# Kernel optimization log

Hardware: AMD Instinct MI355X
Metric: run time of the kernel (lower is better)

Reference implementation:

```python
import jax, jax.numpy as jnp
import numpy as np

NUM_HEADS = 16
HEAD_DIM = 32  # out_ch 512 / 16 heads

def _c(x):
    # last axis holds (real, imag) -> complex64
    return jax.lax.complex(x[..., 0], x[..., 1])

def setup_inputs() -> dict:
    key = jax.random.key(0)
    ks = jax.random.split(key, 9)
    B, S, C = 1, 2048, 512
    mk = lambda k, shp: jax.random.normal(k, shp, dtype=jnp.float32)
    return {
        "Q": mk(ks[0], (B, S, C, 2)),
        "V": mk(ks[1], (B, S, C, 2)),
        "K": mk(ks[2], (B, S, C, 2)),
        "Wq": mk(ks[3], (C, C, 2)) * (1.0 / np.sqrt(C)),
        "bq": mk(ks[4], (C, 2)) * 0.02,
        "Wk": mk(ks[5], (C, C, 2)) * (1.0 / np.sqrt(C)),
        "bk": mk(ks[6], (C, 2)) * 0.02,
        "Wv": mk(ks[7], (C, C, 2)) * (1.0 / np.sqrt(C)),
        "bv": mk(ks[8], (C, 2)) * 0.02,
    }

def _split_heads(x):
    B, S, D = x.shape
    return x.reshape(B, S, NUM_HEADS, HEAD_DIM).transpose(0, 2, 1, 3)  # [B,H,S,d]

def reference(Q, V, K, Wq, bq, Wk, bk, Wv, bv):
    Qc, Kc, Vc = _c(Q), _c(K), _c(V)
    # torch Linear: y = x @ W^T + b, W is [out, in]
    proj = lambda x, W, b: jnp.einsum('bsi,oi->bso', x, _c(W)) + _c(b)
    q = _split_heads(proj(Qc, Wq, bq))  # [B,H,S,d] complex64
    k = _split_heads(proj(Kc, Wk, bk))
    v = _split_heads(proj(Vc, Wv, bv))
    scores = jnp.einsum('bhqd,bhkd->bhqk', q, jnp.conj(k)) / np.sqrt(HEAD_DIM).astype(np.float32)
    weights = jax.nn.softmax(jnp.abs(scores), axis=-1)  # real [B,H,S,S]
    out = jnp.einsum('bhqk,bhkd->bhqd', weights.astype(v.dtype), v)  # complex
    B, H, S, d = out.shape
    out = out.transpose(0, 2, 1, 3).reshape(B, S, H * d)  # [B,S,out_ch]
    return jnp.stack([out.real, out.imag], axis=-1)  # [B,S,out_ch,2] float32
```

## Files before the change

### kernel.cpp

```cpp
#include <hip/hip_runtime.h>
#include <hip/hip_bf16.h>
#include <math.h>

#define S_LEN 2048
#define C_DIM 512
#define NH 16
#define HD 32
#define PLANE_U (NH * S_LEN * HD)

typedef __attribute__((ext_vector_type(8)))  short bf16x8;
typedef __attribute__((ext_vector_type(8)))  unsigned short u16x8;
typedef __attribute__((ext_vector_type(4)))  float f32x4;
typedef __attribute__((ext_vector_type(16))) float f32x16;
typedef __attribute__((ext_vector_type(4)))  unsigned int u32x4;

#if __has_builtin(__builtin_amdgcn_exp2f)
#define EXP2(x) __builtin_amdgcn_exp2f(x)
#else
#define EXP2(x) exp2f(x)
#endif

__device__ __forceinline__ unsigned int pk_bf16(float a, float b) {
    float2 f; f.x = a; f.y = b;
    __hip_bfloat162 t = __float22bfloat162_rn(f);
    return *reinterpret_cast<unsigned int*>(&t);
}

#define PROW 40

__global__ __launch_bounds__(256)
void proj_mfma(const float* __restrict__ Q, const float* __restrict__ V,
               const float* __restrict__ K,
               const float* __restrict__ Wq, const float* __restrict__ bq,
               const float* __restrict__ Wk, const float* __restrict__ bk,
               const float* __restrict__ Wv, const float* __restrict__ bv,
               unsigned short* __restrict__ ws)
{
    const int z = blockIdx.z;
    const float *X, *W, *b;
    if (z == 0)      { X = Q; W = Wq; b = bq; }
    else if (z == 1) { X = K; W = Wk; b = bk; }
    else             { X = V; W = Wv; b = bv; }
    const bool full = (z < 2);

    const int s0 = blockIdx.x * 64;
    const int o0 = blockIdx.y * 64;

    const float2 *Asrc, *Bsrc; int arow0, brow0;
    if (full) { Asrc = (const float2*)W; arow0 = o0; Bsrc = (const float2*)X; brow0 = s0; }
    else      { Asrc = (const float2*)X; arow0 = s0; Bsrc = (const float2*)W; brow0 = o0; }

    __shared__ __align__(16) unsigned short LBrh[64*PROW], LBrl[64*PROW];
    __shared__ __align__(16) unsigned short LBih[64*PROW], LBil[64*PROW];

    const int t    = threadIdx.x;
    const int wave = t >> 6;
    const int lr   = t & 15;
    const int g    = (t & 63) >> 4;
    const int srow = t >> 2;
    const int sk8  = (t & 3) * 8;

    const f32x4 zf = {0.f,0.f,0.f,0.f};
    f32x4 accR[4], accI[4];
    #pragma unroll
    for (int i = 0; i < 4; ++i) { accR[i] = zf; accI[i] = zf; }

    const float4* Arow4 = (const float4*)(Asrc + (size_t)(arow0 + wave*16 + lr)*C_DIM);

    for (int k0 = 0; k0 < C_DIM; k0 += 32) {
        const float4* a4 = Arow4 + ((k0 + g*8) >> 1);
        float4 A0 = a4[0], A1 = a4[1], A2 = a4[2], A3 = a4[3];

        __syncthreads();
        {
            const float4* s4 = (const float4*)(Bsrc + (size_t)(brow0 + srow)*C_DIM + k0 + sk8);
            float4 f0 = s4[0], f1 = s4[1], f2v = s4[2], f3 = s4[3];
            float re[8] = {f0.x,f0.z,f1.x,f1.z,f2v.x,f2v.z,f3.x,f3.z};
            float im[8] = {f0.y,f0.w,f1.y,f1.w,f2v.y,f2v.w,f3.y,f3.w};
            u32x4 rh, ih, rl, il;
            if (full) {
                #pragma unroll
                for (int p2 = 0; p2 < 4; ++p2) {
                    float r0f = re[2*p2], r1f = re[2*p2+1];
                    float i0f = im[2*p2], i1f = im[2*p2+1];
                    unsigned int br0 = __float_as_uint(r0f), br1 = __float_as_uint(r1f);
                    unsigned int bi0 = __float_as_uint(i0f), bi1 = __float_as_uint(i1f);
                    rh[p2] = __builtin_amdgcn_perm(br1, br0, 0x07060302u);
                    ih[p2] = __builtin_amdgcn_perm(bi1, bi0, 0x07060302u);
                    rl[p2] = pk_bf16(r0f - __uint_as_float(br0 & 0xFFFF0000u),
                                     r1f - __uint_as_float(br1 & 0xFFFF0000u));
                    il[p2] = pk_bf16(i0f - __uint_as_float(bi0 & 0xFFFF0000u),
                                     i1f - __uint_as_float(bi1 & 0xFFFF0000u));
                }
            } else {
                #pragma unroll
                for (int p2 = 0; p2 < 4; ++p2) {
                    rh[p2] = pk_bf16(re[2*p2], re[2*p2+1]);
                    ih[p2] = pk_bf16(im[2*p2], im[2*p2+1]);
                }
            }
            int wb = srow*PROW + sk8;
            *(u32x4*)&LBrh[wb] = rh; *(u32x4*)&LBih[wb] = ih;
            if (full) { *(u32x4*)&LBrl[wb] = rl; *(u32x4*)&LBil[wb] = il; }
        }

        bf16x8 aRH, aIH, aRL, aIL;
        {
            float re[8] = {A0.x,A0.z,A1.x,A1.z,A2.x,A2.z,A3.x,A3.z};
            float im[8] = {A0.y,A0.w,A1.y,A1.w,A2.y,A2.w,A3.y,A3.w};
            u32x4 rh, ih, rl, il;
            if (full) {
                #pragma unroll
                for (int p2 = 0; p2 < 4; ++p2) {
                    float r0f = re[2*p2], r1f = re[2*p2+1];
                    float i0f = im[2*p2], i1f = im[2*p2+1];
                    unsigned int br0 = __float_as_uint(r0f), br1 = __float_as_uint(r1f);
                    unsigned int bi0 = __float_as_uint(i0f), bi1 = __float_as_uint(i1f);
                    rh[p2] = __builtin_amdgcn_perm(br1, br0, 0x07060302u);
                    ih[p2] = __builtin_amdgcn_perm(bi1, bi0, 0x07060302u);
                    rl[p2] = pk_bf16(r0f - __uint_as_float(br0 & 0xFFFF0000u),
                                     r1f - __uint_as_float(br1 & 0xFFFF0000u));
                    il[p2] = pk_bf16(i0f - __uint_as_float(bi0 & 0xFFFF0000u),
                                     i1f - __uint_as_float(bi1 & 0xFFFF0000u));
                }
                aRL = *(bf16x8*)&rl; aIL = *(bf16x8*)&il;
            } else {
                #pragma unroll
                for (int p2 = 0; p2 < 4; ++p2) {
                    rh[p2] = pk_bf16(re[2*p2], re[2*p2+1]);
                    ih[p2] = pk_bf16(im[2*p2], im[2*p2+1]);
                }
            }
            aRH = *(bf16x8*)&rh; aIH = *(bf16x8*)&ih;
        }
        bf16x8 aIHn;
        #pragma unroll
        for (int j = 0; j < 8; ++j) aIHn[j] = aIH[j] ^ (short)0x8000;

        __syncthreads();

        if (full) {
            bf16x8 aILn;
            #pragma unroll
            for (int j = 0; j < 8; ++j) aILn[j] = aIL[j] ^ (short)0x8000;

            #pragma unroll
            for (int tile = 0; tile < 4; ++tile) {
                const int bb = (tile*16 + lr)*PROW + g*8;
                bf16x8 bRH = *(const bf16x8*)&LBrh[bb];
                bf16x8 bRL = *(const bf16x8*)&LBrl[bb];
                bf16x8 bIH = *(const bf16x8*)&LBih[bb];
                bf16x8 bIL = *(const bf16x8*)&LBil[bb];
                accR[tile] = __builtin_amdgcn_mfma_f32_16x16x32_bf16(aRH,  bRH, accR[tile], 0,0,0);
                accR[tile] = __builtin_amdgcn_mfma_f32_16x16x32_bf16(aRL,  bRH, accR[tile], 0,0,0);
                accR[tile] = __builtin_amdgcn_mfma_f32_16x16x32_bf16(aRH,  bRL, accR[tile], 0,0,0);
                accR[tile] = __builtin_amdgcn_mfma_f32_16x16x32_bf16(aIHn, bIH, accR[tile], 0,0,0);
                accR[tile] = __builtin_amdgcn_mfma_f32_16x16x32_bf16(aILn, bIH, accR[tile], 0,0,0);
                accR[tile] = __builtin_amdgcn_mfma_f32_16x16x32_bf16(aIHn, bIL, accR[tile], 0,0,0);
                accI[tile] = __builtin_amdgcn_mfma_f32_16x16x32_bf16(aRH,  bIH, accI[tile], 0,0,0);
                accI[tile] = __builtin_amdgcn_mfma_f32_16x16x32_bf16(aRL,  bIH, accI[tile], 0,0,0);
                accI[tile] = __builtin_amdgcn_mfma_f32_16x16x32_bf16(aRH,  bIL, accI[tile], 0,0,0);
                accI[tile] = __builtin_amdgcn_mfma_f32_16x16x32_bf16(aIH,  bRH, accI[tile], 0,0,0);
                accI[tile] = __builtin_amdgcn_mfma_f32_16x16x32_bf16(aIL,  bRH, accI[tile], 0,0,0);
                accI[tile] = __builtin_amdgcn_mfma_f32_16x16x32_bf16(aIH,  bRL, accI[tile], 0,0,0);
            }
        } else {
            #pragma unroll
            for (int tile = 0; tile < 4; ++tile) {
                const int bb = (tile*16 + lr)*PROW + g*8;
                bf16x8 bRH = *(const bf16x8*)&LBrh[bb];
                bf16x8 bIH = *(const bf16x8*)&LBih[bb];
                accR[tile] = __builtin_amdgcn_mfma_f32_16x16x32_bf16(aRH,  bRH, accR[tile], 0,0,0);
                accR[tile] = __builtin_amdgcn_mfma_f32_16x16x32_bf16(aIHn, bIH, accR[tile], 0,0,0);
                accI[tile] = __builtin_amdgcn_mfma_f32_16x16x32_bf16(aRH,  bIH, accI[tile], 0,0,0);
                accI[tile] = __builtin_amdgcn_mfma_f32_16x16x32_bf16(aIH,  bRH, accI[tile], 0,0,0);
            }
        }
    }

    const float2* b2 = (const float2*)b;
    if (z == 0) {
        const float osc = 0.2550348677f;
        unsigned short* pr = ws;
        unsigned short* pi = pr + PLANE_U;
        const int obase = o0 + wave*16 + g*4;
        const int hh = obase >> 5, d0 = obase & 31;
        float bR[4], bI[4];
        #pragma unroll
        for (int r = 0; r < 4; ++r) { float2 bb = b2[obase + r]; bR[r] = bb.x; bI[r] = bb.y; }
        #pragma unroll
        for (int tile = 0; tile < 4; ++tile) {
            int s = s0 + tile*16 + lr;
            size_t idx = ((size_t)hh*S_LEN + s)*HD + d0;
            uint2 pkR, pkI;
            pkR.x = pk_bf16((accR[tile][0]+bR[0])*osc, (accR[tile][1]+bR[1])*osc);
            pkR.y = pk_bf16((accR[tile][2]+bR[2])*osc, (accR[tile][3]+bR[3])*osc);
            pkI.x = pk_bf16((accI[tile][0]+bI[0])*osc, (accI[tile][1]+bI[1])*osc);
            pkI.y = pk_bf16((accI[tile][2]+bI[2])*osc, (accI[tile][3]+bI[3])*osc);
            *(uint2*)&pr[idx] = pkR;
            *(uint2*)&pi[idx] = pkI;
        }
    } else if (z == 1) {
        unsigned short* kf = ws + 2*(size_t)PLANE_U;
        const int obase = o0 + wave*16 + g*4;
        const int hh = obase >> 5, d0 = obase & 31;
        const int frag_re = (d0 >= 16) ? 1 : 0;
        const int bsel    = (d0 & 15) >> 3;
        const int e       = d0 & 7;
        float bR[4], bI[4];
        #pragma unroll
        for (int r = 0; r < 4; ++r) { float2 bb = b2[obase + r]; bR[r] = bb.x; bI[r] = bb.y; }
        #pragma unroll
        for (int tile = 0; tile < 4; ++tile) {
            int s = s0 + tile*16 + lr;
            int c = s >> 5;
            int i = s & 31;
            int r = (i & ~12) | ((i & 4) << 1) | ((i & 8) >> 1);
            int lane = bsel*32 + r;
            size_t base = ((size_t)(hh*64 + c)*4)*512 + lane*8 + e;
            uint2 pkR, pkI;
            pkR.x = pk_bf16(accR[tile][0]+bR[0], accR[tile][1]+bR[1]);
            pkR.y = pk_bf16(accR[tile][2]+bR[2], accR[tile][3]+bR[3]);
            pkI.x = pk_bf16(accI[tile][0]+bI[0], accI[tile][1]+bI[1]);
            pkI.y = pk_bf16(accI[tile][2]+bI[2], accI[tile][3]+bI[3]);
            *(uint2*)&kf[base + (size_t)frag_re*512]       = pkR;
            *(uint2*)&kf[base + (size_t)(2+frag_re)*512]   = pkI;
        }
    } else {
        unsigned short* vf = ws + 4*(size_t)PLANE_U;
        const int sbase = s0 + wave*16 + g*4;
        const int c  = sbase >> 5;
        const int j0 = sbase & 31;
        const int frag_re = (j0 >= 16) ? 1 : 0;
        const int bsel    = (j0 & 15) >> 3;
        const int e       = j0 & 7;
        #pragma unroll
        for (int tile = 0; tile < 4; ++tile) {
            int o = o0 + tile*16 + lr;
            int hh = o >> 5, d = o & 31;
            float2 bb = b2[o];
            int lane = bsel*32 + d;
            size_t base = ((size_t)(hh*64 + c)*4)*512 + lane*8 + e;
            uint2 pkR, pkI;
            pkR.x = pk_bf16(accR[tile][0]+bb.x, accR[tile][1]+bb.x);
            pkR.y = pk_bf16(accR[tile][2]+bb.x, accR[tile][3]+bb.x);
            pkI.x = pk_bf16(accI[tile][0]+bb.y, accI[tile][1]+bb.y);
            pkI.y = pk_bf16(accI[tile][2]+bb.y, accI[tile][3]+bb.y);
            *(uint2*)&vf[base + (size_t)frag_re*512]       = pkR;
            *(uint2*)&vf[base + (size_t)(2+frag_re)*512]   = pkI;
        }
    }
}

#define RROW 33

__global__ __launch_bounds__(256, 4)
void attn_mfma(const unsigned short* __restrict__ ws, float* __restrict__ out)
{
    const int bid   = blockIdx.x;
    const int h     = bid & (NH - 1);
    const int qblk  = bid >> 4;
    const int wave  = threadIdx.x >> 6;
    const int l     = threadIdx.x & 63;
    const int q     = l & 31;
    const int b     = l >> 5;

    const unsigned short* qr = ws + 0*(size_t)PLANE_U + (size_t)h*S_LEN*HD;
    const unsigned short* qi = ws + 1*(size_t)PLANE_U + (size_t)h*S_LEN*HD;
    const unsigned short* kf = ws + 2*(size_t)PLANE_U + ((size_t)h << 17);
    const unsigned short* vf = ws + 4*(size_t)PLANE_U + ((size_t)h << 17);

    const int q0 = qblk * 32;

    bf16x8 bQr_lo = *(const bf16x8*)&qr[(size_t)(q0 + q)*HD + b*8];
    bf16x8 bQr_hi = *(const bf16x8*)&qr[(size_t)(q0 + q)*HD + 16 + b*8];
    bf16x8 bQi_lo = *(const bf16x8*)&qi[(size_t)(q0 + q)*HD + b*8];
    bf16x8 bQi_hi = *(const bf16x8*)&qi[(size_t)(q0 + q)*HD + 16 + b*8];

    __shared__ __align__(16) float2 red[2*32*RROW];

    f32x16 accR, accI;
    #pragma unroll
    for (int r = 0; r < 16; ++r) { accR[r] = 0.f; accI[r] = 0.f; }
    float lsum = 0.f;

    const f32x16 z16 = {0,0,0,0,0,0,0,0,0,0,0,0,0,0,0,0};
    const int kbeg = wave * 512;
    for (int k0 = kbeg; k0 < kbeg + 512; k0 += 32) {
        const size_t fb = (size_t)(k0 >> 5) * 2048 + l*8;

        bf16x8 aVr_lo = *(const bf16x8*)&vf[fb];
        bf16x8 aVr_hi = *(const bf16x8*)&vf[fb + 512];
        bf16x8 aVi_lo = *(const bf16x8*)&vf[fb + 1024];
        bf16x8 aVi_hi = *(const bf16x8*)&vf[fb + 1536];

        bf16x8 aKr_lo = *(const bf16x8*)&kf[fb];
        bf16x8 aKr_hi = *(const bf16x8*)&kf[fb + 512];
        bf16x8 aKi_lo = *(const bf16x8*)&kf[fb + 1024];
        bf16x8 aKi_hi = *(const bf16x8*)&kf[fb + 1536];
        bf16x8 aKin_lo, aKin_hi;
        #pragma unroll
        for (int j = 0; j < 4; ++j) {
            ((unsigned int*)&aKin_lo)[j] = ((const unsigned int*)&aKi_lo)[j] ^ 0x80008000u;
            ((unsigned int*)&aKin_hi)[j] = ((const unsigned int*)&aKi_hi)[j] ^ 0x80008000u;
        }
        f32x16 sR = __builtin_amdgcn_mfma_f32_32x32x16_bf16(aKr_lo,  bQr_lo, z16, 0, 0, 0);
        f32x16 sI = __builtin_amdgcn_mfma_f32_32x32x16_bf16(aKin_lo, bQr_lo, z16, 0, 0, 0);
        sR = __builtin_amdgcn_mfma_f32_32x32x16_bf16(aKr_hi,  bQr_hi, sR, 0, 0, 0);
        sI = __builtin_amdgcn_mfma_f32_32x32x16_bf16(aKin_hi, bQr_hi, sI, 0, 0, 0);
        sR = __builtin_amdgcn_mfma_f32_32x32x16_bf16(aKi_lo,  bQi_lo, sR, 0, 0, 0);
        sI = __builtin_amdgcn_mfma_f32_32x32x16_bf16(aKr_lo,  bQi_lo, sI, 0, 0, 0);
        sR = __builtin_amdgcn_mfma_f32_32x32x16_bf16(aKi_hi,  bQi_hi, sR, 0, 0, 0);
        sI = __builtin_amdgcn_mfma_f32_32x32x16_bf16(aKr_hi,  bQi_hi, sI, 0, 0, 0);
        bf16x8 bP1, bP2;
        unsigned int* p1 = (unsigned int*)&bP1;
        unsigned int* p2 = (unsigned int*)&bP2;
        #pragma unroll
        for (int r2 = 0; r2 < 8; ++r2) {
            int r = 2*r2;
            float v0 = EXP2(__builtin_amdgcn_sqrtf(fmaf(sR[r],   sR[r],   sI[r]*sI[r])));
            float v1 = EXP2(__builtin_amdgcn_sqrtf(fmaf(sR[r+1], sR[r+1], sI[r+1]*sI[r+1])));
            lsum += v0 + v1;
            if (r2 < 4) p1[r2]     = pk_bf16(v0, v1);
            else        p2[r2 - 4] = pk_bf16(v0, v1);
        }
        accR = __builtin_amdgcn_mfma_f32_32x32x16_bf16(aVr_lo, bP1, accR, 0, 0, 0);
        accI = __builtin_amdgcn_mfma_f32_32x32x16_bf16(aVi_lo, bP1, accI, 0, 0, 0);
        accR = __builtin_amdgcn_mfma_f32_32x32x16_bf16(aVr_hi, bP2, accR, 0, 0, 0);
        accI = __builtin_amdgcn_mfma_f32_32x32x16_bf16(aVi_hi, bP2, accI, 0, 0, 0);
    }

    lsum += __shfl_xor(lsum, 32);

    const int rrow = ((wave & 1) * 32 + q) * RROW;
    __syncthreads();
    if (wave < 2) {
        #pragma unroll
        for (int r = 0; r < 16; ++r) {
            int d = (r & 3) + 8*(r >> 2) + 4*b;
            red[rrow + d] = make_float2(accR[r], accI[r]);
        }
        if (b == 0) red[rrow + 32].x = lsum;
    }
    __syncthreads();
    if (wave >= 2) {
        #pragma unroll
        for (int r = 0; r < 16; ++r) {
            int d = (r & 3) + 8*(r >> 2) + 4*b;
            float2 v = red[rrow + d];
            v.x += accR[r]; v.y += accI[r];
            red[rrow + d] = v;
        }
        if (b == 0) red[rrow + 32].x += lsum;
    }
    __syncthreads();

    {
        const int i  = threadIdx.x;
        const int oq = i >> 3;
        const int d0 = (i & 7) * 4;
        float sl = red[oq*RROW + 32].x + red[(32 + oq)*RROW + 32].x;
        float inv = 1.0f / sl;
        float2* o2 = (float2*)out;
        #pragma unroll
        for (int dd = 0; dd < 4; ++dd) {
            int d = d0 + dd;
            float2 v0 = red[oq*RROW + d];
            float2 v1 = red[(32 + oq)*RROW + d];
            o2[(size_t)(q0 + oq)*C_DIM + h*HD + d] =
                make_float2((v0.x + v1.x)*inv, (v0.y + v1.y)*inv);
        }
    }
}

extern "C" void kernel_launch(void* const* d_in, const int* in_sizes, int n_in,
                              void* d_out, int out_size, void* d_ws, size_t ws_size,
                              hipStream_t stream)
{
    const float* Q  = (const float*)d_in[0];
    const float* V  = (const float*)d_in[1];
    const float* K  = (const float*)d_in[2];
    const float* Wq = (const float*)d_in[3];
    const float* bq = (const float*)d_in[4];
    const float* Wk = (const float*)d_in[5];
    const float* bk = (const float*)d_in[6];
    const float* Wv = (const float*)d_in[7];
    const float* bv = (const float*)d_in[8];
    unsigned short* ws = (unsigned short*)d_ws;
    float* out = (float*)d_out;

    dim3 gp(S_LEN/64, C_DIM/64, 3);
    proj_mfma<<<gp, 256, 0, stream>>>(Q, V, K, Wq, bq, Wk, bk, Wv, bv, ws);

    attn_mfma<<<dim3(64*NH), 256, 0, stream>>>(ws, out);
}
```

Measured before the change: 81.72 us.

## Pre-convert weights to bf16 split planes and shrink projection seq tile

Adds a separate kernel that converts Wq/Wk/Wv into bf16 hi/lo planes once per call, so the projection kernel loads ready-made MFMA operands instead of re-splitting fp32 weights in every block. The projection's sequence tile drops from 64 to 32 rows, doubling the block count. The V projection now always uses weights as the A operand, which changes its output scatter to scalar 16-bit stores. The cost is an extra launch, extra workspace traffic, and less reuse of each weight fetch per block.

```diff
diff --git a/kernel.cpp b/kernel.cpp
--- a/kernel.cpp
+++ b/kernel.cpp
@@ -7,12 +7,14 @@
 #define NH 16
 #define HD 32
 #define PLANE_U (NH * S_LEN * HD)
+#define WPL 262144
 
 typedef __attribute__((ext_vector_type(8)))  short bf16x8;
 typedef __attribute__((ext_vector_type(8)))  unsigned short u16x8;
 typedef __attribute__((ext_vector_type(4)))  float f32x4;
 typedef __attribute__((ext_vector_type(16))) float f32x16;
 typedef __attribute__((ext_vector_type(4)))  unsigned int u32x4;
+typedef __attribute__((ext_vector_type(2)))  unsigned int u32x2;
 
 #if __has_builtin(__builtin_amdgcn_exp2f)
 #define EXP2(x) __builtin_amdgcn_exp2f(x)
@@ -26,61 +28,118 @@
     return *reinterpret_cast<unsigned int*>(&t);
 }
 
+__global__ __launch_bounds__(256)
+void wcvt(const float* __restrict__ Wq, const float* __restrict__ Wk,
+          const float* __restrict__ Wv, unsigned short* __restrict__ ws)
+{
+    const int tid = blockIdx.x*256 + threadIdx.x;
+    const int z   = tid >> 15;
+    const int rem = tid & 32767;
+    const int row = rem >> 6;
+    const int kc  = (rem & 63) * 8;
+    const float2* w2 = (const float2*)(z == 0 ? Wq : (z == 1 ? Wk : Wv));
+    const float4* s4 = (const float4*)(w2 + (size_t)row*C_DIM + kc);
+    float4 f0 = s4[0], f1 = s4[1], f2v = s4[2], f3 = s4[3];
+    float re[8] = {f0.x,f0.z,f1.x,f1.z,f2v.x,f2v.z,f3.x,f3.z};
+    float im[8] = {f0.y,f0.w,f1.y,f1.w,f2v.y,f2v.w,f3.y,f3.w};
+    unsigned short* wf = ws + 6*(size_t)PLANE_U;
+    const size_t off = (size_t)row*C_DIM + kc;
+    if (z < 2) {
+        u32x4 rh, ih, rl, il;
+        #pragma unroll
+        for (int p2 = 0; p2 < 4; ++p2) {
+            float r0f = re[2*p2], r1f = re[2*p2+1];
+            float i0f = im[2*p2], i1f = im[2*p2+1];
+            unsigned int br0 = __float_as_uint(r0f), br1 = __float_as_uint(r1f);
+            unsigned int bi0 = __float_as_uint(i0f), bi1 = __float_as_uint(i1f);
+            rh[p2] = __builtin_amdgcn_perm(br1, br0, 0x07060302u);
+            ih[p2] = __builtin_amdgcn_perm(bi1, bi0, 0x07060302u);
+            rl[p2] = pk_bf16(r0f - __uint_as_float(br0 & 0xFFFF0000u),
+                             r1f - __uint_as_float(br1 & 0xFFFF0000u));
+            il[p2] = pk_bf16(i0f - __uint_as_float(bi0 & 0xFFFF0000u),
+                             i1f - __uint_as_float(bi1 & 0xFFFF0000u));
+        }
+        const size_t pb = (size_t)z*4*WPL;
+        *(u32x4*)&wf[pb + 0*WPL + off] = rh;
+        *(u32x4*)&wf[pb + 1*WPL + off] = rl;
+        *(u32x4*)&wf[pb + 2*WPL + off] = ih;
+        *(u32x4*)&wf[pb + 3*WPL + off] = il;
+    } else {
+        u32x4 rh, ih;
+        #pragma unroll
+        for (int p2 = 0; p2 < 4; ++p2) {
+            rh[p2] = pk_bf16(re[2*p2], re[2*p2+1]);
+            ih[p2] = pk_bf16(im[2*p2], im[2*p2+1]);
+        }
+        *(u32x4*)&wf[(size_t)8*WPL + off] = rh;
+        *(u32x4*)&wf[(size_t)9*WPL + off] = ih;
+    }
+}
+
 #define PROW 40
 
 __global__ __launch_bounds__(256)
 void proj_mfma(const float* __restrict__ Q, const float* __restrict__ V,
                const float* __restrict__ K,
-               const float* __restrict__ Wq, const float* __restrict__ bq,
-               const float* __restrict__ Wk, const float* __restrict__ bk,
-               const float* __restrict__ Wv, const float* __restrict__ bv,
+               const float* __restrict__ bq, const float* __restrict__ bk,
+               const float* __restrict__ bv,
                unsigned short* __restrict__ ws)
 {
     const int z = blockIdx.z;
-    const float *X, *W, *b;
-    if (z == 0)      { X = Q; W = Wq; b = bq; }
-    else if (z == 1) { X = K; W = Wk; b = bk; }
-    else             { X = V; W = Wv; b = bv; }
+    const float *X, *b;
+    if (z == 0)      { X = Q; b = bq; }
+    else if (z == 1) { X = K; b = bk; }
+    else             { X = V; b = bv; }
     const bool full = (z < 2);
 
-    const int s0 = blockIdx.x * 64;
+    const int s0 = blockIdx.x * 32;
     const int o0 = blockIdx.y * 64;
 
-    const float2 *Asrc, *Bsrc; int arow0, brow0;
-    if (full) { Asrc = (const float2*)W; arow0 = o0; Bsrc = (const float2*)X; brow0 = s0; }
-    else      { Asrc = (const float2*)X; arow0 = s0; Bsrc = (const float2*)W; brow0 = o0; }
-
-    __shared__ __align__(16) unsigned short LBrh[64*PROW], LBrl[64*PROW];
-    __shared__ __align__(16) unsigned short LBih[64*PROW], LBil[64*PROW];
+    const float2* Bsrc = (const float2*)X;
+    const unsigned short* wf = ws + 6*(size_t)PLANE_U;
+    const size_t pb = full ? (size_t)z*4*WPL : (size_t)8*WPL;
+
+    __shared__ __align__(16) unsigned short LBrh[32*PROW], LBrl[32*PROW];
+    __shared__ __align__(16) unsigned short LBih[32*PROW], LBil[32*PROW];
 
     const int t    = threadIdx.x;
     const int wave = t >> 6;
     const int lr   = t & 15;
     const int g    = (t & 63) >> 4;
-    const int srow = t >> 2;
-    const int sk8  = (t & 3) * 8;
+    const int srow = t >> 3;
+    const int skc  = (t & 7) * 4;
 
     const f32x4 zf = {0.f,0.f,0.f,0.f};
-    f32x4 accR[4], accI[4];
+    f32x4 accR[2], accI[2];
     #pragma unroll
-    for (int i = 0; i < 4; ++i) { accR[i] = zf; accI[i] = zf; }
-
-    const float4* Arow4 = (const float4*)(Asrc + (size_t)(arow0 + wave*16 + lr)*C_DIM);
+    for (int i = 0; i < 2; ++i) { accR[i] = zf; accI[i] = zf; }
+
+    const size_t arow = (size_t)(o0 + wave*16 + lr) * C_DIM;
 
     for (int k0 = 0; k0 < C_DIM; k0 += 32) {
-        const float4* a4 = Arow4 + ((k0 + g*8) >> 1);
-        float4 A0 = a4[0], A1 = a4[1], A2 = a4[2], A3 = a4[3];
+        const size_t ak = arow + k0 + g*8;
+        bf16x8 aRH = *(const bf16x8*)&wf[pb + 0*WPL + ak];
+        bf16x8 aIH = *(const bf16x8*)&wf[pb + (full ? 2 : 1)*WPL + ak];
+        bf16x8 aRL, aIL;
+        if (full) {
+            aRL = *(const bf16x8*)&wf[pb + 1*WPL + ak];
+            aIL = *(const bf16x8*)&wf[pb + 3*WPL + ak];
+        }
+        bf16x8 aIHn;
+        #pragma unroll
+        for (int j = 0; j < 4; ++j)
+            ((unsigned int*)&aIHn)[j] = ((const unsigned int*)&aIH)[j] ^ 0x80008000u;
 
         __syncthreads();
         {
-            const float4* s4 = (const float4*)(Bsrc + (size_t)(brow0 + srow)*C_DIM + k0 + sk8);
-            float4 f0 = s4[0], f1 = s4[1], f2v = s4[2], f3 = s4[3];
-            float re[8] = {f0.x,f0.z,f1.x,f1.z,f2v.x,f2v.z,f3.x,f3.z};
-            float im[8] = {f0.y,f0.w,f1.y,f1.w,f2v.y,f2v.w,f3.y,f3.w};
-            u32x4 rh, ih, rl, il;
+            const float4* s4 = (const float4*)(Bsrc + (size_t)(s0 + srow)*C_DIM + k0 + skc);
+            float4 f0 = s4[0], f1 = s4[1];
+            float re[4] = {f0.x, f0.z, f1.x, f1.z};
+            float im[4] = {f0.y, f0.w, f1.y, f1.w};
+            u32x2 rh, ih, rl, il;
             if (full) {
                 #pragma unroll
-                for (int p2 = 0; p2 < 4; ++p2) {
+                for (int p2 = 0; p2 < 2; ++p2) {
                     float r0f = re[2*p2], r1f = re[2*p2+1];
                     float i0f = im[2*p2], i1f = im[2*p2+1];
                     unsigned int br0 = __float_as_uint(r0f), br1 = __float_as_uint(r1f);
@@ -94,58 +153,25 @@
                 }
             } else {
                 #pragma unroll
-                for (int p2 = 0; p2 < 4; ++p2) {
+                for (int p2 = 0; p2 < 2; ++p2) {
                     rh[p2] = pk_bf16(re[2*p2], re[2*p2+1]);
                     ih[p2] = pk_bf16(im[2*p2], im[2*p2+1]);
                 }
             }
-            int wb = srow*PROW + sk8;
-            *(u32x4*)&LBrh[wb] = rh; *(u32x4*)&LBih[wb] = ih;
-            if (full) { *(u32x4*)&LBrl[wb] = rl; *(u32x4*)&LBil[wb] = il; }
-        }
-
-        bf16x8 aRH, aIH, aRL, aIL;
-        {
-            float re[8] = {A0.x,A0.z,A1.x,A1.z,A2.x,A2.z,A3.x,A3.z};
-            float im[8] = {A0.y,A0.w,A1.y,A1.w,A2.y,A2.w,A3.y,A3.w};
-            u32x4 rh, ih, rl, il;
-            if (full) {
-                #pragma unroll
-                for (int p2 = 0; p2 < 4; ++p2) {
-                    float r0f = re[2*p2], r1f = re[2*p2+1];
-                    float i0f = im[2*p2], i1f = im[2*p2+1];
-                    unsigned int br0 = __float_as_uint(r0f), br1 = __float_as_uint(r1f);
-                    unsigned int bi0 = __float_as_uint(i0f), bi1 = __float_as_uint(i1f);
-                    rh[p2] = __builtin_amdgcn_perm(br1, br0, 0x07060302u);
-                    ih[p2] = __builtin_amdgcn_perm(bi1, bi0, 0x07060302u);
-                    rl[p2] = pk_bf16(r0f - __uint_as_float(br0 & 0xFFFF0000u),
-                                     r1f - __uint_as_float(br1 & 0xFFFF0000u));
-                    il[p2] = pk_bf16(i0f - __uint_as_float(bi0 & 0xFFFF0000u),
-                                     i1f - __uint_as_float(bi1 & 0xFFFF0000u));
-                }
-                aRL = *(bf16x8*)&rl; aIL = *(bf16x8*)&il;
-            } else {
-                #pragma unroll
-                for (int p2 = 0; p2 < 4; ++p2) {
-                    rh[p2] = pk_bf16(re[2*p2], re[2*p2+1]);
-                    ih[p2] = pk_bf16(im[2*p2], im[2*p2+1]);
-                }
-            }
-            aRH = *(bf16x8*)&rh; aIH = *(bf16x8*)&ih;
-        }
-        bf16x8 aIHn;
-        #pragma unroll
-        for (int j = 0; j < 8; ++j) aIHn[j] = aIH[j] ^ (short)0x8000;
-
+            int wb = srow*PROW + skc;
+            *(u32x2*)&LBrh[wb] = rh; *(u32x2*)&LBih[wb] = ih;
+            if (full) { *(u32x2*)&LBrl[wb] = rl; *(u32x2*)&LBil[wb] = il; }
+        }
         __syncthreads();
 
         if (full) {
             bf16x8 aILn;
             #pragma unroll
-            for (int j = 0; j < 8; ++j) aILn[j] = aIL[j] ^ (short)0x8000;
+            for (int j = 0; j < 4; ++j)
+                ((unsigned int*)&aILn)[j] = ((const unsigned int*)&aIL)[j] ^ 0x80008000u;
 
             #pragma unroll
-            for (int tile = 0; tile < 4; ++tile) {
+            for (int tile = 0; tile < 2; ++tile) {
                 const int bb = (tile*16 + lr)*PROW + g*8;
                 bf16x8 bRH = *(const bf16x8*)&LBrh[bb];
                 bf16x8 bRL = *(const bf16x8*)&LBrl[bb];
@@ -166,7 +192,7 @@
             }
         } else {
             #pragma unroll
-            for (int tile = 0; tile < 4; ++tile) {
+            for (int tile = 0; tile < 2; ++tile) {
                 const int bb = (tile*16 + lr)*PROW + g*8;
                 bf16x8 bRH = *(const bf16x8*)&LBrh[bb];
                 bf16x8 bIH = *(const bf16x8*)&LBih[bb];
@@ -179,17 +205,18 @@
     }
 
     const float2* b2 = (const float2*)b;
+    const int obase = o0 + wave*16 + g*4;
+    const int hh = obase >> 5, d0 = obase & 31;
+    float bR[4], bI[4];
+    #pragma unroll
+    for (int r = 0; r < 4; ++r) { float2 bb = b2[obase + r]; bR[r] = bb.x; bI[r] = bb.y; }
+
     if (z == 0) {
         const float osc = 0.2550348677f;
         unsigned short* pr = ws;
         unsigned short* pi = pr + PLANE_U;
-        const int obase = o0 + wave*16 + g*4;
-        const int hh = obase >> 5, d0 = obase & 31;
-        float bR[4], bI[4];
-        #pragma unroll
-        for (int r = 0; r < 4; ++r) { float2 bb = b2[obase + r]; bR[r] = bb.x; bI[r] = bb.y; }
-        #pragma unroll
-        for (int tile = 0; tile < 4; ++tile) {
+        #pragma unroll
+        for (int tile = 0; tile < 2; ++tile) {
             int s = s0 + tile*16 + lr;
             size_t idx = ((size_t)hh*S_LEN + s)*HD + d0;
             uint2 pkR, pkI;
@@ -202,19 +229,13 @@
         }
     } else if (z == 1) {
         unsigned short* kf = ws + 2*(size_t)PLANE_U;
-        const int obase = o0 + wave*16 + g*4;
-        const int hh = obase >> 5, d0 = obase & 31;
         const int frag_re = (d0 >= 16) ? 1 : 0;
         const int bsel    = (d0 & 15) >> 3;
         const int e       = d0 & 7;
-        float bR[4], bI[4];
-        #pragma unroll
-        for (int r = 0; r < 4; ++r) { float2 bb = b2[obase + r]; bR[r] = bb.x; bI[r] = bb.y; }
-        #pragma unroll
-        for (int tile = 0; tile < 4; ++tile) {
-            int s = s0 + tile*16 + lr;
-            int c = s >> 5;
-            int i = s & 31;
+        const int c       = s0 >> 5;
+        #pragma unroll
+        for (int tile = 0; tile < 2; ++tile) {
+            int i = tile*16 + lr;
             int r = (i & ~12) | ((i & 4) << 1) | ((i & 8) >> 1);
             int lane = bsel*32 + r;
             size_t base = ((size_t)(hh*64 + c)*4)*512 + lane*8 + e;
@@ -223,31 +244,27 @@
             pkR.y = pk_bf16(accR[tile][2]+bR[2], accR[tile][3]+bR[3]);
             pkI.x = pk_bf16(accI[tile][0]+bI[0], accI[tile][1]+bI[1]);
             pkI.y = pk_bf16(accI[tile][2]+bI[2], accI[tile][3]+bI[3]);
-            *(uint2*)&kf[base + (size_t)frag_re*512]       = pkR;
-            *(uint2*)&kf[base + (size_t)(2+frag_re)*512]   = pkI;
+            *(uint2*)&kf[base + (size_t)frag_re*512]     = pkR;
+            *(uint2*)&kf[base + (size_t)(2+frag_re)*512] = pkI;
         }
     } else {
         unsigned short* vf = ws + 4*(size_t)PLANE_U;
-        const int sbase = s0 + wave*16 + g*4;
-        const int c  = sbase >> 5;
-        const int j0 = sbase & 31;
-        const int frag_re = (j0 >= 16) ? 1 : 0;
-        const int bsel    = (j0 & 15) >> 3;
-        const int e       = j0 & 7;
-        #pragma unroll
-        for (int tile = 0; tile < 4; ++tile) {
-            int o = o0 + tile*16 + lr;
-            int hh = o >> 5, d = o & 31;
-            float2 bb = b2[o];
-            int lane = bsel*32 + d;
-            size_t base = ((size_t)(hh*64 + c)*4)*512 + lane*8 + e;
-            uint2 pkR, pkI;
-            pkR.x = pk_bf16(accR[tile][0]+bb.x, accR[tile][1]+bb.x);
-            pkR.y = pk_bf16(accR[tile][2]+bb.x, accR[tile][3]+bb.x);
-            pkI.x = pk_bf16(accI[tile][0]+bb.y, accI[tile][1]+bb.y);
-            pkI.y = pk_bf16(accI[tile][2]+bb.y, accI[tile][3]+bb.y);
-            *(uint2*)&vf[base + (size_t)frag_re*512]       = pkR;
-            *(uint2*)&vf[base + (size_t)(2+frag_re)*512]   = pkI;
+        const int c = s0 >> 5;
+        #pragma unroll
+        for (int tile = 0; tile < 2; ++tile) {
+            const int frag_re = tile;
+            const int bsel    = lr >> 3;
+            const int e       = lr & 7;
+            const size_t cb   = ((size_t)(hh*64 + c)*4)*512;
+            #pragma unroll
+            for (int r = 0; r < 4; ++r) {
+                int lane = bsel*32 + d0 + r;
+                size_t base = cb + (size_t)lane*8 + e;
+                vf[base + (size_t)frag_re*512]     =
+                    (unsigned short)pk_bf16(accR[tile][r]+bR[r], 0.f);
+                vf[base + (size_t)(2+frag_re)*512] =
+                    (unsigned short)pk_bf16(accI[tile][r]+bI[r], 0.f);
+            }
         }
     }
 }
@@ -312,6 +329,7 @@
         sI = __builtin_amdgcn_mfma_f32_32x32x16_bf16(aKr_lo,  bQi_lo, sI, 0, 0, 0);
         sR = __builtin_amdgcn_mfma_f32_32x32x16_bf16(aKi_hi,  bQi_hi, sR, 0, 0, 0);
         sI = __builtin_amdgcn_mfma_f32_32x32x16_bf16(aKr_hi,  bQi_hi, sI, 0, 0, 0);
+
         bf16x8 bP1, bP2;
         unsigned int* p1 = (unsigned int*)&bP1;
         unsigned int* p2 = (unsigned int*)&bP2;
@@ -389,8 +407,7 @@
     unsigned short* ws = (unsigned short*)d_ws;
     float* out = (float*)d_out;
 
-    dim3 gp(S_LEN/64, C_DIM/64, 3);
-    proj_mfma<<<gp, 256, 0, stream>>>(Q, V, K, Wq, bq, Wk, bk, Wv, bv, ws);
-
+    wcvt<<<384, 256, 0, stream>>>(Wq, Wk, Wv, ws);
+    proj_mfma<<<dim3(S_LEN/32, C_DIM/64, 3), 256, 0, stream>>>(Q, V, K, bq, bk, bv, ws);
     attn_mfma<<<dim3(64*NH), 256, 0, stream>>>(ws, out);
 }
```

Measured after the change: 93.92 us. 1.15x slower.
